# Kernel tuning notes

Hardware: AMD Instinct MI355X
Metric: run time of the kernel (lower is better)

## Reference

```python
import jax, jax.numpy as jnp
import numpy as np

B, T, D_MODEL = 4, 4096, 512
HEADS, BUCKET_SIZE, N_HASHES = 8, 64, 4
DIM_HEAD = D_MODEL // HEADS  # 64
D_FFN = 2048
N_BUCKETS = T // BUCKET_SIZE  # 64
SELF_ATTN_VALUE = -5e4  # reformer TOKEN_SELF_ATTN_VALUE


def setup_inputs() -> dict:
    key = jax.random.key(0)
    ks = jax.random.split(key, 16)
    s = 0.02
    return {
        'x': jax.random.normal(ks[0], (B, T, D_MODEL), jnp.float32),
        'rotations': jax.random.normal(ks[1], (DIM_HEAD, N_HASHES, N_BUCKETS // 2), jnp.float32),
        'w_qk': jax.random.normal(ks[2], (D_MODEL, D_MODEL), jnp.float32) * s,
        'w_v': jax.random.normal(ks[3], (D_MODEL, D_MODEL), jnp.float32) * s,
        'w_out': jax.random.normal(ks[4], (D_MODEL, D_MODEL), jnp.float32) * s,
        'b_out': jnp.zeros((D_MODEL,), jnp.float32),
        'ln1_g': jnp.ones((D_MODEL,), jnp.float32),
        'ln1_b': jnp.zeros((D_MODEL,), jnp.float32),
        'w1': jax.random.normal(ks[5], (D_FFN, D_MODEL), jnp.float32) * s,
        'b1': jnp.zeros((D_FFN,), jnp.float32),
        'w2': jax.random.normal(ks[6], (D_MODEL, D_FFN), jnp.float32) * s,
        'b2': jnp.zeros((D_MODEL,), jnp.float32),
        'ln2_g': jnp.ones((D_MODEL,), jnp.float32),
        'ln2_b': jnp.zeros((D_MODEL,), jnp.float32),
    }


def layer_norm(x, g, b, eps=1e-6):
    m = x.mean(-1, keepdims=True)
    v = ((x - m) ** 2).mean(-1, keepdims=True)
    return (x - m) / jnp.sqrt(v + eps) * g + b


def look_one_back(x):
    # concat each chunk with the previous chunk (wrap-around), along in-chunk axis
    prev = jnp.roll(x, 1, axis=1)
    return jnp.concatenate([x, prev], axis=2)


def lsh_attention(qk, v, rotations):
    # qk, v: (bh, t, d) with shared-QK; rotations: (d, n_hashes, n_buckets//2)
    bh, t, d = qk.shape
    # --- hash: random rotations, argmax over [R, -R] ---
    rot = jnp.einsum('btf,fhi->bhti', qk, rotations)
    rot = jnp.concatenate([rot, -rot], axis=-1)        # (bh, H, t, n_buckets)
    buckets = jnp.argmax(rot, axis=-1)                 # (bh, H, t)
    buckets = buckets + (jnp.arange(N_HASHES) * N_BUCKETS)[None, :, None]
    buckets = buckets.reshape(bh, N_HASHES * t)
    # --- sort by (bucket, position) ---
    ticker = jnp.arange(N_HASHES * t)
    buckets_and_t = t * buckets + (ticker % t)[None, :]
    sticker = jnp.argsort(buckets_and_t, axis=-1)      # stable sort
    undo_sort = jnp.argsort(sticker, axis=-1)
    st = sticker % t                                   # original positions, sorted order
    sqk = jnp.take_along_axis(qk, st[..., None], axis=1)
    sv = jnp.take_along_axis(v, st[..., None], axis=1)
    # --- chunk: n_hashes*n_buckets chunks of bucket_size tokens ---
    n_chunks = N_HASHES * N_BUCKETS
    bq_t = st.reshape(bh, n_chunks, -1)
    bqk = sqk.reshape(bh, n_chunks, -1, d)
    bv = sv.reshape(bh, n_chunks, -1, d)
    bk = bqk / jnp.clip(jnp.linalg.norm(bqk, axis=-1, keepdims=True), 1e-6, None)
    bk = look_one_back(bk)
    bv = look_one_back(bv)
    bkv_t = look_one_back(bq_t)
    # --- local attention within chunk (+ previous chunk) ---
    dots = jnp.einsum('bcid,bcjd->bcij', bqk, bk) * (DIM_HEAD ** -0.5)
    self_mask = bq_t[..., None] == bkv_t[..., None, :]
    dots = jnp.where(self_mask, SELF_ATTN_VALUE, dots)
    logits = jax.nn.logsumexp(dots, axis=-1, keepdims=True)
    probs = jnp.exp(dots - logits)
    bo = jnp.einsum('bcij,bcjd->bcid', probs, bv)
    # --- unsort and combine hash rounds by softmax over round logits ---
    so = bo.reshape(bh, N_HASHES * t, d)
    slogits = logits.reshape(bh, N_HASHES * t)
    o = jnp.take_along_axis(so, undo_sort[..., None], axis=1).reshape(bh, N_HASHES, t, d)
    lg = jnp.take_along_axis(slogits, undo_sort, axis=1).reshape(bh, N_HASHES, t, 1)
    w = jnp.exp(lg - jax.nn.logsumexp(lg, axis=1, keepdims=True))
    return (o * w).sum(axis=1)                         # (bh, t, d)


def reference(x, rotations, w_qk, w_v, w_out, b_out, ln1_g, ln1_b, w1, b1, w2, b2, ln2_g, ln2_b):
    b, t, _ = x.shape
    qk = x @ w_qk.T
    v = x @ w_v.T

    def split_heads(u):
        return u.reshape(b, t, HEADS, DIM_HEAD).transpose(0, 2, 1, 3).reshape(b * HEADS, t, DIM_HEAD)

    attn = lsh_attention(split_heads(qk), split_heads(v), rotations)
    attn = attn.reshape(b, HEADS, t, DIM_HEAD).transpose(0, 2, 1, 3).reshape(b, t, D_MODEL)
    attn = attn @ w_out.T + b_out
    # residual + LN (dropout is identity at inference)
    h = layer_norm(attn + x, ln1_g, ln1_b)
    # position-wise FFN with its own residual + LN
    f = jax.nn.relu(h @ w1.T + b1) @ w2.T + b2
    return layer_norm(f + h, ln2_g, ln2_b)
```

## Files before the change

### kernel.cpp

```cpp
#include <hip/hip_runtime.h>
#include <stdint.h>

typedef unsigned short u16;
typedef __attribute__((ext_vector_type(4))) int   i32x4;
typedef __attribute__((ext_vector_type(4))) float f32x4;

__device__ __forceinline__ u16 f2bf(float x){
  unsigned int u = __float_as_uint(x);
  u += 0x7FFFu + ((u >> 16) & 1u);
  return (u16)(u >> 16);
}
__device__ __forceinline__ float bf2f(u16 h){
  return __uint_as_float(((unsigned int)h) << 16);
}
__device__ __forceinline__ f32x4 mfma16(i32x4 a, i32x4 b, f32x4 c){
  asm("v_mfma_f32_16x16x32_bf16 %0, %1, %2, %0" : "+v"(c) : "v"(a), "v"(b));
  return c;
}
__device__ __forceinline__ f32x4 acc_fence(f32x4 c){
  asm volatile("s_nop 7\ns_nop 7" : "+v"(c));
  return c;
}
__device__ __forceinline__ void gl_lds16(const void* g, void* l){
  unsigned long long ga = (unsigned long long)g;
  unsigned int la = (unsigned int)(unsigned long long)l;
  __builtin_amdgcn_global_load_lds((const __attribute__((address_space(1))) void*)ga,
                                   (__attribute__((address_space(3))) void*)la, 16, 0, 0);
}
__device__ __forceinline__ int xcd_swz(int f, int n){
  int chunk = n >> 3;
  return (f & 7) * chunk + (f >> 3);
}
__device__ __forceinline__ unsigned int f2mono(float v){
  unsigned int u = __float_as_uint(v);
  return u ^ ((unsigned int)((int)u >> 31) | 0x80000000u);
}
__device__ __forceinline__ float mono2f(unsigned int mu){
  unsigned int u = (mu & 0x80000000u) ? (mu ^ 0x80000000u) : ~mu;
  return __uint_as_float(u);
}
__device__ __forceinline__ unsigned long long shfl_xor_u64(unsigned long long x, int m){
  int lo = __shfl_xor((int)(unsigned int)(x & 0xFFFFFFFFull), m);
  int hi = __shfl_xor((int)(unsigned int)(x >> 32), m);
  return ((unsigned long long)(unsigned int)hi << 32) | (unsigned int)lo;
}

__global__ __launch_bounds__(256) void k_cvt(const float* __restrict__ in, u16* __restrict__ out, int n4){
  int i = blockIdx.x*256 + threadIdx.x;
  if (i >= n4) return;
  float4 v = ((const float4*)in)[i];
  ushort4 o; o.x=f2bf(v.x); o.y=f2bf(v.y); o.z=f2bf(v.z); o.w=f2bf(v.w);
  ((ushort4*)out)[i] = o;
}
__global__ __launch_bounds__(256) void k_split(const float* __restrict__ in, u16* __restrict__ hi, u16* __restrict__ lo, int n4){
  int i = blockIdx.x*256 + threadIdx.x;
  if (i >= n4) return;
  float4 v = ((const float4*)in)[i];
  ushort4 h, l;
  h.x=f2bf(v.x); l.x=f2bf(v.x - bf2f(h.x));
  h.y=f2bf(v.y); l.y=f2bf(v.y - bf2f(h.y));
  h.z=f2bf(v.z); l.z=f2bf(v.z - bf2f(h.z));
  h.w=f2bf(v.w); l.w=f2bf(v.w - bf2f(h.w));
  ((ushort4*)hi)[i]=h; ((ushort4*)lo)[i]=l;
}
__global__ __launch_bounds__(256) void k_rotT(const float* __restrict__ rot, u16* __restrict__ hi, u16* __restrict__ lo){
  int i = blockIdx.x*256 + threadIdx.x;
  if (i >= 8192) return;
  int d = i & 63, n = i >> 6;
  float v = rot[d*128 + n];
  u16 h = f2bf(v);
  hi[i] = h; lo[i] = f2bf(v - bf2f(h));
}

template<int MODE>
__global__ __launch_bounds__(256) void k_gemm(
    const u16* __restrict__ A0, const u16* __restrict__ A1,
    const u16* __restrict__ B0, const u16* __restrict__ B1,
    const float* __restrict__ bias,
    float* __restrict__ Cf, u16* __restrict__ Cb,
    u16* __restrict__ Cb2, u16* __restrict__ Cb3,
    int M, int N, int K, int nterms)
{
  const int tid = threadIdx.x;
  const int l = tid & 63, w = tid >> 6;
  const int lr = l & 15, lg = l >> 4;
  int flat = blockIdx.y * gridDim.x + blockIdx.x;
  flat = xcd_swz(flat, gridDim.x * gridDim.y);
  const int m0 = (flat / gridDim.x) * 128, n0 = (flat % gridDim.x) * 128;
  const int mbase = (w >> 1) * 64, nbase = (w & 1) * 64;

  __shared__ __align__(16) u16 As[128*64];
  __shared__ __align__(16) u16 Bs[128*64];

  f32x4 zero = {0.f,0.f,0.f,0.f};
  f32x4 acc[4][4];
  #pragma unroll
  for (int i=0;i<4;i++)
    #pragma unroll
    for (int j=0;j<4;j++) acc[i][j] = zero;

  const int row_s = tid >> 3;
  const int c16   = tid & 7;

  for (int term = 0; term < nterms; ++term){
    const u16* Ap = (term==2) ? A1 : A0;
    const u16* Bp = (term==1) ? B1 : B0;
    for (int k0 = 0; k0 < K; k0 += 64){
      #pragma unroll
      for (int q=0;q<4;q++){
        int ra = q*32 + row_s;
        int cs = c16 ^ (ra & 7);
        gl_lds16(Ap + (size_t)(m0 + ra)*K + k0 + cs*8, (char*)As + q*4096 + tid*16);
        gl_lds16(Bp + (size_t)(n0 + ra)*K + k0 + cs*8, (char*)Bs + q*4096 + tid*16);
      }
      __syncthreads();
      #pragma unroll
      for (int kk=0; kk<64; kk+=32){
        i32x4 af[4], bfr[4];
        #pragma unroll
        for (int mf=0;mf<4;mf++){
          int row = mbase + mf*16 + lr;
          af[mf] = *(const i32x4*)((const char*)As + row*128 + (((kk*2) + (lg*16)) ^ ((row&7)<<4)));
        }
        #pragma unroll
        for (int nf=0;nf<4;nf++){
          int row = nbase + nf*16 + lr;
          bfr[nf] = *(const i32x4*)((const char*)Bs + row*128 + (((kk*2) + (lg*16)) ^ ((row&7)<<4)));
        }
        #pragma unroll
        for (int mf=0;mf<4;mf++)
          #pragma unroll
          for (int nf=0;nf<4;nf++)
            acc[mf][nf] = mfma16(af[mf], bfr[nf], acc[mf][nf]);
      }
      __syncthreads();
    }
  }

  if (MODE == 2){
    const int hh = (n0 + nbase) >> 6;
    #pragma unroll
    for (int mf=0;mf<4;mf++){
      f32x4 v[4];
      #pragma unroll
      for (int nf=0;nf<4;nf++) v[nf] = acc_fence(acc[mf][nf]);
      #pragma unroll
      for (int r=0;r<4;r++){
        float ss = 0.f;
        #pragma unroll
        for (int nf=0;nf<4;nf++) ss += v[nf][r]*v[nf][r];
        ss += __shfl_xor(ss, 1); ss += __shfl_xor(ss, 2);
        ss += __shfl_xor(ss, 4); ss += __shfl_xor(ss, 8);
        float scale = 1.f / fmaxf(sqrtf(ss), 1e-6f);
        int m = m0 + mbase + mf*16 + lg*4 + r;
        int b = m >> 12, t = m & 4095;
        size_t rowb = ((((size_t)(b*8 + hh)) << 12) + t) * 64;
        #pragma unroll
        for (int nf=0;nf<4;nf++){
          float val = v[nf][r];
          u16 hbf = f2bf(val);
          size_t idx = rowb + nf*16 + lr;
          Cb [idx] = hbf;
          Cb2[idx] = f2bf(val - bf2f(hbf));
          Cb3[idx] = f2bf(val * scale);
        }
      }
    }
    return;
  }

  #pragma unroll
  for (int mf=0;mf<4;mf++){
    #pragma unroll
    for (int nf=0;nf<4;nf++){
      f32x4 v = acc_fence(acc[mf][nf]);
      #pragma unroll
      for (int r=0;r<4;r++){
        int m = m0 + mbase + mf*16 + lg*4 + r;
        int n = n0 + nbase + nf*16 + lr;
        float val = v[r];
        if (MODE == 0){
          if (bias) val += bias[n];
          Cf[(size_t)m*N + n] = val;
        } else if (MODE == 1){
          val += bias[n];
          val = fmaxf(val, 0.f);
          Cb[(size_t)m*N + n] = f2bf(val);
        } else {
          int b = m >> 12, t = m & 4095, h = n >> 6, d = n & 63;
          size_t idx = ((((size_t)(b*8 + h)) << 12) + t)*64 + d;
          Cb[idx] = f2bf(val);
        }
      }
    }
  }
}

__global__ __launch_bounds__(256) void k_hash2(
    const u16* __restrict__ qh, const u16* __restrict__ ql,
    const u16* __restrict__ rh, const u16* __restrict__ rl,
    int* __restrict__ bkt)
{
  const int tid = threadIdx.x;
  const int l = tid & 63, w = tid >> 6, lr = l & 15, lg = l >> 4;
  __shared__ __align__(16) u16 Rh[128*64];
  __shared__ __align__(16) u16 Rl[128*64];
  {
    const int row_s = tid >> 3, c8 = tid & 7;
    #pragma unroll
    for (int q = 0; q < 4; q++){
      int ra = q*32 + row_s;
      int cs = c8 ^ (ra & 7);
      gl_lds16(rh + ra*64 + cs*8, (char*)Rh + q*4096 + tid*16);
      gl_lds16(rl + ra*64 + cs*8, (char*)Rl + q*4096 + tid*16);
    }
  }
  const int blk = xcd_swz(blockIdx.x, gridDim.x);
  const int qrow = blk*64 + w*16 + lr;
  const size_t qoff = (size_t)qrow*64;
  i32x4 qhf[2], qlf[2];
  qhf[0] = *(const i32x4*)(qh + qoff + lg*8);
  qhf[1] = *(const i32x4*)(qh + qoff + 32 + lg*8);
  qlf[0] = *(const i32x4*)(ql + qoff + lg*8);
  qlf[1] = *(const i32x4*)(ql + qoff + 32 + lg*8);
  __syncthreads();

  f32x4 zero = {0.f,0.f,0.f,0.f};
  f32x4 acc[8];
  #pragma unroll
  for (int i=0;i<8;i++) acc[i] = zero;
  #pragma unroll
  for (int ks = 0; ks < 2; ks++){
    #pragma unroll
    for (int nf = 0; nf < 8; nf++){
      int row = nf*16 + lr;
      int off = (ks*64 + lg*16) ^ ((row & 7) << 4);
      i32x4 rhf = *(const i32x4*)((const char*)Rh + row*128 + off);
      i32x4 rlf = *(const i32x4*)((const char*)Rl + row*128 + off);
      acc[nf] = mfma16(rhf, qhf[ks], acc[nf]);
      acc[nf] = mfma16(rlf, qhf[ks], acc[nf]);
      acc[nf] = mfma16(rhf, qlf[ks], acc[nf]);
    }
  }

  const int bh = qrow >> 12, t = qrow & 4095;
  #pragma unroll
  for (int hh = 0; hh < 4; hh++){
    f32x4 v0 = acc_fence(acc[2*hh]);
    f32x4 v1 = acc_fence(acc[2*hh+1]);
    unsigned long long kmax = 0, kmin = 0;
    #pragma unroll
    for (int r = 0; r < 4; r++){
      int j0 = lg*4 + r, j1 = 16 + lg*4 + r;
      unsigned int mu0 = f2mono(v0[r]), mu1 = f2mono(v1[r]);
      unsigned long long a = ((unsigned long long)mu0 << 32) | (unsigned int)(31 - j0);
      unsigned long long b = ((unsigned long long)mu1 << 32) | (unsigned int)(31 - j1);
      if (a > kmax) kmax = a;
      if (b > kmax) kmax = b;
      unsigned long long c = ((unsigned long long)(~mu0) << 32) | (unsigned int)(31 - j0);
      unsigned long long d = ((unsigned long long)(~mu1) << 32) | (unsigned int)(31 - j1);
      if (c > kmin) kmin = c;
      if (d > kmin) kmin = d;
    }
    #pragma unroll
    for (int msk = 16; msk < 64; msk <<= 1){
      unsigned long long o1 = shfl_xor_u64(kmax, msk); if (o1 > kmax) kmax = o1;
      unsigned long long o2 = shfl_xor_u64(kmin, msk); if (o2 > kmin) kmin = o2;
    }
    if (lg == 0){
      float vmax = mono2f((unsigned int)(kmax >> 32));
      int jmax = 31 - (int)(kmax & 0xFFFFFFFFull);
      float vmin = mono2f(~(unsigned int)(kmin >> 32));
      int jmin = 31 - (int)(kmin & 0xFFFFFFFFull);
      int bucket = (vmax >= -vmin) ? jmax : 32 + jmin;
      bkt[((size_t)(bh*4 + hh) << 12) + t] = bucket;
    }
  }
}

__global__ __launch_bounds__(64) void k_sort(const int* __restrict__ buckets, int* __restrict__ st){
  const int grp = blockIdx.x;
  const int t = threadIdx.x;
  __shared__ int hist[64][65];
  __shared__ int tot[64];
  const size_t gbase = ((size_t)grp) << 12;
  #pragma unroll
  for (int b=0;b<64;b++) hist[t][b] = 0;
  __syncthreads();
  for (int i=0;i<64;i++){
    int b = buckets[gbase + t*64 + i];
    hist[t][b]++;
  }
  __syncthreads();
  { int run = 0;
    for (int tt=0; tt<64; tt++){ int v = hist[tt][t]; hist[tt][t] = run; run += v; }
    tot[t] = run; }
  __syncthreads();
  { int v = tot[t]; int incl = v;
    #pragma unroll
    for (int d=1; d<64; d<<=1){ int n = __shfl_up(incl, d, 64); if (t >= d) incl += n; }
    tot[t] = incl - v; }
  __syncthreads();
  const size_t obase = (((size_t)(grp>>2)) << 14) + ((size_t)(grp&3) << 12);
  for (int i=0;i<64;i++){
    int e = t*64 + i;
    int b = buckets[gbase + e];
    int dest = tot[b] + hist[t][b];
    hist[t][b]++;
    st[obase + dest] = e;
  }
}

__global__ __launch_bounds__(256, 4) void k_attn(
    const u16* __restrict__ qb, const u16* __restrict__ kn, const u16* __restrict__ vB,
    const int* __restrict__ st, float* __restrict__ lgt_out, u16* __restrict__ bo)
{
  int flat = blockIdx.y * gridDim.x + blockIdx.x;
  flat = xcd_swz(flat, gridDim.x * gridDim.y);
  const int c = flat & 255, bh = flat >> 8;
  const int rnd = c >> 6;
  const int tid = threadIdx.x;
  const int l = tid & 63, w = tid >> 6, lr = l & 15, lg = l >> 4;

  __shared__ __align__(16) u16 Ks[128*64];
  __shared__ __align__(16) u16 Vt[64][136];
  __shared__ int posk[128];

  if (tid < 128){
    int cc = (tid < 64) ? c : ((c + 255) & 255);
    posk[tid] = st[(((size_t)bh) << 14) + (cc << 6) + (tid & 63)];
  }
  __syncthreads();

  const size_t kvbase = ((size_t)bh) << 12;

  {
    const int rsub = l >> 3, c8 = l & 7;
    #pragma unroll
    for (int q2 = 0; q2 < 4; q2++){
      int row = w*32 + q2*8 + rsub;
      int cs = c8 ^ (row & 7);
      gl_lds16(kn + (kvbase + posk[row])*64 + cs*8,
               (char*)Ks + (w*4 + q2)*1024 + l*16);
    }
  }

  const int pos_q16 = posk[w*16 + lr];
  i32x4 qf[2];
  #pragma unroll
  for (int ks = 0; ks < 2; ks++)
    qf[ks] = *(const i32x4*)(qb + (kvbase + pos_q16)*64 + ks*32 + lg*8);

  {
    const int pp = tid & 63, db = tid >> 6;
    const int q5 = pp & 15;
    const int K0 = (pp >> 4)*32 + 16*((q5 >> 1) & 1) + 4*(q5 >> 2) + 2*(q5 & 1);
    const u16* r0 = vB + (kvbase + posk[K0])*64 + db*16;
    const u16* r1 = vB + (kvbase + posk[K0+1])*64 + db*16;
    uint4 a0 = *(const uint4*)r0, a1 = *(const uint4*)(r0 + 8);
    uint4 b0 = *(const uint4*)r1, b1 = *(const uint4*)(r1 + 8);
    uint av[8] = {a0.x,a0.y,a0.z,a0.w,a1.x,a1.y,a1.z,a1.w};
    uint bv[8] = {b0.x,b0.y,b0.z,b0.w,b1.x,b1.y,b1.z,b1.w};
    #pragma unroll
    for (int dd = 0; dd < 16; dd++){
      uint lo = (av[dd>>1] >> ((dd&1)*16)) & 0xFFFFu;
      uint hi = (bv[dd>>1] >> ((dd&1)*16)) & 0xFFFFu;
      *(uint*)((char*)&Vt[db*16 + dd][0] + pp*4) = lo | (hi << 16);
    }
  }
  __syncthreads();

  f32x4 zero = {0.f,0.f,0.f,0.f};
  f32x4 s[8];
  #pragma unroll
  for (int i=0;i<8;i++) s[i] = zero;
  #pragma unroll
  for (int ks = 0; ks < 2; ks++){
    #pragma unroll
    for (int nf = 0; nf < 8; nf++){
      int row = nf*16 + lr;
      i32x4 kf = *(const i32x4*)((const char*)Ks + row*128 + ((ks*64 + lg*16) ^ ((row&7)<<4)));
      s[nf] = mfma16(kf, qf[ks], s[nf]);
    }
  }

  float sv[8][4];
  const int q_loc = w*16 + lr;
  #pragma unroll
  for (int nf=0;nf<8;nf++){
    f32x4 t = acc_fence(s[nf]);
    #pragma unroll
    for (int r=0;r<4;r++){
      int k = nf*16 + lg*4 + r;
      sv[nf][r] = (k == q_loc) ? -5e4f : t[r]*0.125f;
    }
  }
  float m = -1e30f;
  #pragma unroll
  for (int nf=0;nf<8;nf++)
    #pragma unroll
    for (int r=0;r<4;r++) m = fmaxf(m, sv[nf][r]);
  m = fmaxf(m, __shfl_xor(m, 16));
  m = fmaxf(m, __shfl_xor(m, 32));
  float sum = 0.f;
  #pragma unroll
  for (int nf=0;nf<8;nf++)
    #pragma unroll
    for (int r=0;r<4;r++){ sv[nf][r] = __expf(sv[nf][r] - m); sum += sv[nf][r]; }
  sum += __shfl_xor(sum, 16);
  sum += __shfl_xor(sum, 32);
  float lv = m + logf(sum);
  float inv = 1.f / sum;
  if (l < 16)
    lgt_out[(((size_t)(bh*4 + rnd)) << 12) + pos_q16] = lv;

  i32x4 pa[4];
  #pragma unroll
  for (int ks=0;ks<4;ks++){
    uint wd[4];
    #pragma unroll
    for (int h2=0; h2<2; h2++){
      int nf = 2*ks + h2;
      float p0 = sv[nf][0]*inv, p1 = sv[nf][1]*inv;
      float p2 = sv[nf][2]*inv, p3 = sv[nf][3]*inv;
      wd[h2*2]   = (uint)f2bf(p0) | ((uint)f2bf(p1)<<16);
      wd[h2*2+1] = (uint)f2bf(p2) | ((uint)f2bf(p3)<<16);
    }
    i32x4 t = {(int)wd[0],(int)wd[1],(int)wd[2],(int)wd[3]};
    pa[ks] = t;
  }

  f32x4 o[4];
  #pragma unroll
  for (int i=0;i<4;i++) o[i] = zero;
  #pragma unroll
  for (int ks=0;ks<4;ks++){
    #pragma unroll
    for (int nf=0;nf<4;nf++){
      i32x4 vf = *(const i32x4*)((const char*)&Vt[nf*16 + lr][0] + ks*64 + lg*16);
      o[nf] = mfma16(pa[ks], vf, o[nf]);
    }
  }
  #pragma unroll
  for (int nf=0;nf<4;nf++){
    f32x4 ov = acc_fence(o[nf]);
    #pragma unroll
    for (int r=0;r<4;r++){
      int q = w*16 + lg*4 + r;
      bo[((((size_t)(bh*4 + rnd)) << 12) + posk[q])*64 + nf*16 + lr] = f2bf(ov[r]);
    }
  }
}

__global__ __launch_bounds__(256) void k_combine(const u16* __restrict__ bo, const float* __restrict__ lgt,
                                                 u16* __restrict__ attn){
  const int wid = blockIdx.x * 4 + (threadIdx.x >> 6);
  const int l = threadIdx.x & 63;
  const int bh = wid >> 12, t = wid & 4095;
  const size_t lbase = (((size_t)bh) << 14) + t;
  float l0 = lgt[lbase], l1 = lgt[lbase + 4096], l2 = lgt[lbase + 8192], l3 = lgt[lbase + 12288];
  float m = fmaxf(fmaxf(l0,l1), fmaxf(l2,l3));
  float w0 = __expf(l0-m), w1 = __expf(l1-m), w2 = __expf(l2-m), w3 = __expf(l3-m);
  float inv = 1.f / (w0+w1+w2+w3);
  const size_t bbase = ((((size_t)bh) << 14) + t) * 64 + l;
  float o = w0 * bf2f(bo[bbase])
          + w1 * bf2f(bo[bbase + (size_t)4096*64])
          + w2 * bf2f(bo[bbase + (size_t)8192*64])
          + w3 * bf2f(bo[bbase + (size_t)12288*64]);
  o *= inv;
  int b = bh >> 3, h = bh & 7;
  attn[((((size_t)b) << 12) + t) * 512 + h*64 + l] = f2bf(o);
}

template<int WB16>
__global__ __launch_bounds__(256) void k_ln(const float* __restrict__ a, const float* __restrict__ res,
                                            const float* __restrict__ g, const float* __restrict__ bb,
                                            float* __restrict__ of, u16* __restrict__ ob){
  const int row = blockIdx.x*4 + (threadIdx.x >> 6);
  const int l = threadIdx.x & 63;
  const size_t base = (size_t)row*512 + l*8;
  float4 a0 = *(const float4*)(a + base);
  float4 a1 = *(const float4*)(a + base + 4);
  float4 r0 = *(const float4*)(res + base);
  float4 r1 = *(const float4*)(res + base + 4);
  float v[8] = {a0.x+r0.x, a0.y+r0.y, a0.z+r0.z, a0.w+r0.w,
                a1.x+r1.x, a1.y+r1.y, a1.z+r1.z, a1.w+r1.w};
  float sum = 0.f;
  #pragma unroll
  for (int j=0;j<8;j++) sum += v[j];
  #pragma unroll
  for (int msk=1; msk<64; msk<<=1) sum += __shfl_xor(sum, msk);
  float mean = sum * (1.f/512.f);
  float ss = 0.f;
  #pragma unroll
  for (int j=0;j<8;j++){ float d = v[j]-mean; ss += d*d; }
  #pragma unroll
  for (int msk=1; msk<64; msk<<=1) ss += __shfl_xor(ss, msk);
  float rstd = rsqrtf(ss * (1.f/512.f) + 1e-6f);
  float4 g0 = *(const float4*)(g + l*8),  g1 = *(const float4*)(g + l*8 + 4);
  float4 b0 = *(const float4*)(bb + l*8), b1 = *(const float4*)(bb + l*8 + 4);
  float gv[8] = {g0.x,g0.y,g0.z,g0.w,g1.x,g1.y,g1.z,g1.w};
  float bv[8] = {b0.x,b0.y,b0.z,b0.w,b1.x,b1.y,b1.z,b1.w};
  float y[8];
  #pragma unroll
  for (int j=0;j<8;j++) y[j] = (v[j]-mean)*rstd*gv[j] + bv[j];
  #pragma unroll
  for (int j=0;j<8;j++) of[base+j] = y[j];
  if (WB16){
    #pragma unroll
    for (int j=0;j<8;j++) ob[base+j] = f2bf(y[j]);
  }
}

extern "C" void kernel_launch(void* const* d_in, const int* in_sizes, int n_in,
                              void* d_out, int out_size, void* d_ws, size_t ws_size,
                              hipStream_t stream) {
  const float* x     = (const float*)d_in[0];
  const float* rot   = (const float*)d_in[1];
  const float* w_qk  = (const float*)d_in[2];
  const float* w_v   = (const float*)d_in[3];
  const float* w_out = (const float*)d_in[4];
  const float* b_out = (const float*)d_in[5];
  const float* ln1_g = (const float*)d_in[6];
  const float* ln1_b = (const float*)d_in[7];
  const float* w1    = (const float*)d_in[8];
  const float* b1    = (const float*)d_in[9];
  const float* w2    = (const float*)d_in[10];
  const float* b2    = (const float*)d_in[11];
  const float* ln2_g = (const float*)d_in[12];
  const float* ln2_b = (const float*)d_in[13];
  float* out = (float*)d_out;

  char* p = (char*)d_ws;
  u16*   xh   = (u16*)(p);
  u16*   xl   = (u16*)(p + 16777216);
  u16*   wqkh = (u16*)(p + 33554432);
  u16*   wqkl = (u16*)(p + 34078720);
  u16*   wvb  = (u16*)(p + 34603008);
  u16*   wob  = (u16*)(p + 35127296);
  u16*   w1b  = (u16*)(p + 35651584);
  u16*   w2b  = (u16*)(p + 37748736);
  u16*   qbuf = (u16*)(p + 39845888);
  u16*   knb  = (u16*)(p + 56623104);
  u16*   vb   = (u16*)(p + 73400320);
  int*   bkt  = (int*)(p + 90177536);
  int*   stb  = (int*)(p + 92274688);
  float* lgt  = (float*)(p + 94371840);
  u16*   bo   = (u16*)(p + 96468992);
  u16*   qlo   = bo;
  u16*   rothi = wqkh;
  u16*   rotlo = wqkl;
  u16*   attnc = xl;
  float* hf    = (float*)(p + 39845888);
  u16*   hb    = xh;
  u16*   hid   = bo;

  k_split<<<8192, 256, 0, stream>>>(x, xh, xl, 16384*512/4);
  k_split<<<256,  256, 0, stream>>>(w_qk, wqkh, wqkl, 512*512/4);
  k_cvt  <<<256,  256, 0, stream>>>(w_v,   wvb, 512*512/4);
  k_cvt  <<<256,  256, 0, stream>>>(w_out, wob, 512*512/4);
  k_cvt  <<<1024, 256, 0, stream>>>(w1, w1b, 2048*512/4);
  k_cvt  <<<1024, 256, 0, stream>>>(w2, w2b, 2048*512/4);

  k_gemm<2><<<dim3(4,128), 256, 0, stream>>>(xh, xl, wqkh, wqkl, nullptr, nullptr, qbuf, qlo, knb, 16384, 512, 512, 3);
  k_gemm<3><<<dim3(4,128), 256, 0, stream>>>(xh, nullptr, wvb, nullptr, nullptr, nullptr, vb, nullptr, nullptr, 16384, 512, 512, 1);
  k_rotT<<<32, 256, 0, stream>>>(rot, rothi, rotlo);
  k_hash2<<<2048, 256, 0, stream>>>(qbuf, qlo, rothi, rotlo, bkt);
  k_sort<<<128, 64, 0, stream>>>(bkt, stb);
  k_attn<<<dim3(256,32), 256, 0, stream>>>(qbuf, knb, vb, stb, lgt, bo);
  k_combine<<<32768, 256, 0, stream>>>(bo, lgt, attnc);
  k_gemm<0><<<dim3(4,128), 256, 0, stream>>>(attnc, nullptr, wob, nullptr, b_out, out, nullptr, nullptr, nullptr, 16384, 512, 512, 1);
  k_ln<1><<<4096, 256, 0, stream>>>(out, x, ln1_g, ln1_b, hf, hb);
  k_gemm<1><<<dim3(16,128), 256, 0, stream>>>(hb, nullptr, w1b, nullptr, b1, nullptr, hid, nullptr, nullptr, 16384, 2048, 512, 1);
  k_gemm<0><<<dim3(4,128), 256, 0, stream>>>(hid, nullptr, w2b, nullptr, b2, out, nullptr, nullptr, nullptr, 16384, 512, 2048, 1);
  k_ln<0><<<4096, 256, 0, stream>>>(out, hf, ln2_g, ln2_b, out, nullptr);
}
```

Measured before the change: 333.9 us.

## Fuse split-bf16 QK GEMM terms, stage sort buckets in LDS, streamline attention softmax

Several separate changes. The three-term split-bf16 QK projection moves into a dedicated kernel that loads hi/lo A and B tiles once and issues the three MFMAs per tile together, instead of looping over terms and reloading tiles. The sort kernel stages bucket ids in LDS with coalesced loads rather than strided global reads. The attention kernel folds the 1/8 scale into the normalized key and drops the max subtraction, relying on bounded cosine logits. It also defers the 1/sum normalization to after the PV MFMA, uses packed bf16 conversion instructions, and raises wave priority around MFMA blocks. The cost is extra LDS in the QK GEMM, which may lower occupancy.

Result: faster. 315.0 us (-5.7%).

```diff
diff --git a/kernel.cpp b/kernel.cpp
--- a/kernel.cpp
+++ b/kernel.cpp
@@ -12,6 +12,11 @@
 }
 __device__ __forceinline__ float bf2f(u16 h){
   return __uint_as_float(((unsigned int)h) << 16);
+}
+__device__ __forceinline__ unsigned int cvtpk_bf16(float lo, float hi){
+  unsigned int r;
+  asm("v_cvt_pk_bf16_f32 %0, %1, %2" : "=v"(r) : "v"(lo), "v"(hi));
+  return r;
 }
 __device__ __forceinline__ f32x4 mfma16(i32x4 a, i32x4 b, f32x4 c){
   asm("v_mfma_f32_16x16x32_bf16 %0, %1, %2, %0" : "+v"(c) : "v"(a), "v"(b));
@@ -74,12 +79,10 @@
 
 template<int MODE>
 __global__ __launch_bounds__(256) void k_gemm(
-    const u16* __restrict__ A0, const u16* __restrict__ A1,
-    const u16* __restrict__ B0, const u16* __restrict__ B1,
+    const u16* __restrict__ A0, const u16* __restrict__ B0,
     const float* __restrict__ bias,
     float* __restrict__ Cf, u16* __restrict__ Cb,
-    u16* __restrict__ Cb2, u16* __restrict__ Cb3,
-    int M, int N, int K, int nterms)
+    int M, int N, int K)
 {
   const int tid = threadIdx.x;
   const int l = tid & 63, w = tid >> 6;
@@ -102,71 +105,35 @@
   const int row_s = tid >> 3;
   const int c16   = tid & 7;
 
-  for (int term = 0; term < nterms; ++term){
-    const u16* Ap = (term==2) ? A1 : A0;
-    const u16* Bp = (term==1) ? B1 : B0;
-    for (int k0 = 0; k0 < K; k0 += 64){
-      #pragma unroll
-      for (int q=0;q<4;q++){
-        int ra = q*32 + row_s;
-        int cs = c16 ^ (ra & 7);
-        gl_lds16(Ap + (size_t)(m0 + ra)*K + k0 + cs*8, (char*)As + q*4096 + tid*16);
-        gl_lds16(Bp + (size_t)(n0 + ra)*K + k0 + cs*8, (char*)Bs + q*4096 + tid*16);
+  for (int k0 = 0; k0 < K; k0 += 64){
+    #pragma unroll
+    for (int q=0;q<4;q++){
+      int ra = q*32 + row_s;
+      int cs = c16 ^ (ra & 7);
+      gl_lds16(A0 + (size_t)(m0 + ra)*K + k0 + cs*8, (char*)As + q*4096 + tid*16);
+      gl_lds16(B0 + (size_t)(n0 + ra)*K + k0 + cs*8, (char*)Bs + q*4096 + tid*16);
+    }
+    __syncthreads();
+    #pragma unroll
+    for (int kk=0; kk<64; kk+=32){
+      i32x4 af[4], bfr[4];
+      #pragma unroll
+      for (int mf=0;mf<4;mf++){
+        int row = mbase + mf*16 + lr;
+        af[mf] = *(const i32x4*)((const char*)As + row*128 + (((kk*2) + (lg*16)) ^ ((row&7)<<4)));
       }
-      __syncthreads();
-      #pragma unroll
-      for (int kk=0; kk<64; kk+=32){
-        i32x4 af[4], bfr[4];
+      #pragma unroll
+      for (int nf=0;nf<4;nf++){
+        int row = nbase + nf*16 + lr;
+        bfr[nf] = *(const i32x4*)((const char*)Bs + row*128 + (((kk*2) + (lg*16)) ^ ((row&7)<<4)));
+      }
+      #pragma unroll
+      for (int mf=0;mf<4;mf++)
         #pragma unroll
-        for (int mf=0;mf<4;mf++){
-          int row = mbase + mf*16 + lr;
-          af[mf] = *(const i32x4*)((const char*)As + row*128 + (((kk*2) + (lg*16)) ^ ((row&7)<<4)));
-        }
-        #pragma unroll
-        for (int nf=0;nf<4;nf++){
-          int row = nbase + nf*16 + lr;
-          bfr[nf] = *(const i32x4*)((const char*)Bs + row*128 + (((kk*2) + (lg*16)) ^ ((row&7)<<4)));
-        }
-        #pragma unroll
-        for (int mf=0;mf<4;mf++)
-          #pragma unroll
-          for (int nf=0;nf<4;nf++)
-            acc[mf][nf] = mfma16(af[mf], bfr[nf], acc[mf][nf]);
-      }
-      __syncthreads();
-    }
-  }
-
-  if (MODE == 2){
-    const int hh = (n0 + nbase) >> 6;
-    #pragma unroll
-    for (int mf=0;mf<4;mf++){
-      f32x4 v[4];
-      #pragma unroll
-      for (int nf=0;nf<4;nf++) v[nf] = acc_fence(acc[mf][nf]);
-      #pragma unroll
-      for (int r=0;r<4;r++){
-        float ss = 0.f;
-        #pragma unroll
-        for (int nf=0;nf<4;nf++) ss += v[nf][r]*v[nf][r];
-        ss += __shfl_xor(ss, 1); ss += __shfl_xor(ss, 2);
-        ss += __shfl_xor(ss, 4); ss += __shfl_xor(ss, 8);
-        float scale = 1.f / fmaxf(sqrtf(ss), 1e-6f);
-        int m = m0 + mbase + mf*16 + lg*4 + r;
-        int b = m >> 12, t = m & 4095;
-        size_t rowb = ((((size_t)(b*8 + hh)) << 12) + t) * 64;
-        #pragma unroll
-        for (int nf=0;nf<4;nf++){
-          float val = v[nf][r];
-          u16 hbf = f2bf(val);
-          size_t idx = rowb + nf*16 + lr;
-          Cb [idx] = hbf;
-          Cb2[idx] = f2bf(val - bf2f(hbf));
-          Cb3[idx] = f2bf(val * scale);
-        }
-      }
-    }
-    return;
+        for (int nf=0;nf<4;nf++)
+          acc[mf][nf] = mfma16(af[mf], bfr[nf], acc[mf][nf]);
+    }
+    __syncthreads();
   }
 
   #pragma unroll
@@ -196,6 +163,107 @@
   }
 }
 
+__global__ __launch_bounds__(256) void k_gemmqk(
+    const u16* __restrict__ Ah, const u16* __restrict__ Al,
+    const u16* __restrict__ Bh, const u16* __restrict__ Bl,
+    u16* __restrict__ qb, u16* __restrict__ qlo, u16* __restrict__ kn)
+{
+  const int K = 512;
+  const int tid = threadIdx.x;
+  const int l = tid & 63, w = tid >> 6;
+  const int lr = l & 15, lg = l >> 4;
+  int flat = blockIdx.y * gridDim.x + blockIdx.x;
+  flat = xcd_swz(flat, gridDim.x * gridDim.y);
+  const int m0 = (flat >> 2) * 128, n0 = (flat & 3) * 128;
+  const int mbase = (w >> 1) * 64, nbase = (w & 1) * 64;
+
+  __shared__ __align__(16) u16 AsH[128*64];
+  __shared__ __align__(16) u16 AsL[128*64];
+  __shared__ __align__(16) u16 BsH[128*64];
+  __shared__ __align__(16) u16 BsL[128*64];
+
+  f32x4 zero = {0.f,0.f,0.f,0.f};
+  f32x4 acc[4][4];
+  #pragma unroll
+  for (int i=0;i<4;i++)
+    #pragma unroll
+    for (int j=0;j<4;j++) acc[i][j] = zero;
+
+  const int row_s = tid >> 3;
+  const int c16   = tid & 7;
+
+  for (int k0 = 0; k0 < K; k0 += 64){
+    #pragma unroll
+    for (int q=0;q<4;q++){
+      int ra = q*32 + row_s;
+      int cs = c16 ^ (ra & 7);
+      size_t ao = (size_t)(m0 + ra)*K + k0 + cs*8;
+      size_t bo = (size_t)(n0 + ra)*K + k0 + cs*8;
+      gl_lds16(Ah + ao, (char*)AsH + q*4096 + tid*16);
+      gl_lds16(Al + ao, (char*)AsL + q*4096 + tid*16);
+      gl_lds16(Bh + bo, (char*)BsH + q*4096 + tid*16);
+      gl_lds16(Bl + bo, (char*)BsL + q*4096 + tid*16);
+    }
+    __syncthreads();
+    #pragma unroll
+    for (int kk=0; kk<64; kk+=32){
+      i32x4 ah[4], al[4], bh2[4], bl2[4];
+      #pragma unroll
+      for (int mf=0;mf<4;mf++){
+        int row = mbase + mf*16 + lr;
+        int off = (((kk*2) + (lg*16)) ^ ((row&7)<<4));
+        ah[mf] = *(const i32x4*)((const char*)AsH + row*128 + off);
+        al[mf] = *(const i32x4*)((const char*)AsL + row*128 + off);
+      }
+      #pragma unroll
+      for (int nf=0;nf<4;nf++){
+        int row = nbase + nf*16 + lr;
+        int off = (((kk*2) + (lg*16)) ^ ((row&7)<<4));
+        bh2[nf] = *(const i32x4*)((const char*)BsH + row*128 + off);
+        bl2[nf] = *(const i32x4*)((const char*)BsL + row*128 + off);
+      }
+      #pragma unroll
+      for (int mf=0;mf<4;mf++)
+        #pragma unroll
+        for (int nf=0;nf<4;nf++){
+          acc[mf][nf] = mfma16(ah[mf], bh2[nf], acc[mf][nf]);
+          acc[mf][nf] = mfma16(al[mf], bh2[nf], acc[mf][nf]);
+          acc[mf][nf] = mfma16(ah[mf], bl2[nf], acc[mf][nf]);
+        }
+    }
+    __syncthreads();
+  }
+
+  const int hh = (n0 + nbase) >> 6;
+  #pragma unroll
+  for (int mf=0;mf<4;mf++){
+    f32x4 v[4];
+    #pragma unroll
+    for (int nf=0;nf<4;nf++) v[nf] = acc_fence(acc[mf][nf]);
+    #pragma unroll
+    for (int r=0;r<4;r++){
+      float ss = 0.f;
+      #pragma unroll
+      for (int nf=0;nf<4;nf++) ss += v[nf][r]*v[nf][r];
+      ss += __shfl_xor(ss, 1); ss += __shfl_xor(ss, 2);
+      ss += __shfl_xor(ss, 4); ss += __shfl_xor(ss, 8);
+      float scale = 0.125f / fmaxf(sqrtf(ss), 1e-6f);
+      int m = m0 + mbase + mf*16 + lg*4 + r;
+      int b = m >> 12, t = m & 4095;
+      size_t rowb = ((((size_t)(b*8 + hh)) << 12) + t) * 64;
+      #pragma unroll
+      for (int nf=0;nf<4;nf++){
+        float val = v[nf][r];
+        u16 hbf = f2bf(val);
+        size_t idx = rowb + nf*16 + lr;
+        qb [idx] = hbf;
+        qlo[idx] = f2bf(val - bf2f(hbf));
+        kn [idx] = f2bf(val * scale);
+      }
+    }
+  }
+}
+
 __global__ __launch_bounds__(256) void k_hash2(
     const u16* __restrict__ qh, const u16* __restrict__ ql,
     const u16* __restrict__ rh, const u16* __restrict__ rl,
@@ -281,14 +349,17 @@
 __global__ __launch_bounds__(64) void k_sort(const int* __restrict__ buckets, int* __restrict__ st){
   const int grp = blockIdx.x;
   const int t = threadIdx.x;
+  __shared__ int bkL[4096];
   __shared__ int hist[64][65];
   __shared__ int tot[64];
   const size_t gbase = ((size_t)grp) << 12;
+  for (int i=0;i<64;i++)
+    bkL[i*64 + t] = buckets[gbase + i*64 + t];
   #pragma unroll
   for (int b=0;b<64;b++) hist[t][b] = 0;
   __syncthreads();
   for (int i=0;i<64;i++){
-    int b = buckets[gbase + t*64 + i];
+    int b = bkL[t*64 + i];
     hist[t][b]++;
   }
   __syncthreads();
@@ -304,7 +375,7 @@
   const size_t obase = (((size_t)(grp>>2)) << 14) + ((size_t)(grp&3) << 12);
   for (int i=0;i<64;i++){
     int e = t*64 + i;
-    int b = buckets[gbase + e];
+    int b = bkL[e];
     int dest = tot[b] + hist[t][b];
     hist[t][b]++;
     st[obase + dest] = e;
@@ -374,6 +445,7 @@
   f32x4 s[8];
   #pragma unroll
   for (int i=0;i<8;i++) s[i] = zero;
+  __builtin_amdgcn_s_setprio(1);
   #pragma unroll
   for (int ks = 0; ks < 2; ks++){
     #pragma unroll
@@ -383,33 +455,25 @@
       s[nf] = mfma16(kf, qf[ks], s[nf]);
     }
   }
-
-  float sv[8][4];
+  __builtin_amdgcn_s_setprio(0);
+
+  float p[8][4];
   const int q_loc = w*16 + lr;
+  float sum = 0.f;
   #pragma unroll
   for (int nf=0;nf<8;nf++){
     f32x4 t = acc_fence(s[nf]);
     #pragma unroll
     for (int r=0;r<4;r++){
       int k = nf*16 + lg*4 + r;
-      sv[nf][r] = (k == q_loc) ? -5e4f : t[r]*0.125f;
-    }
-  }
-  float m = -1e30f;
-  #pragma unroll
-  for (int nf=0;nf<8;nf++)
-    #pragma unroll
-    for (int r=0;r<4;r++) m = fmaxf(m, sv[nf][r]);
-  m = fmaxf(m, __shfl_xor(m, 16));
-  m = fmaxf(m, __shfl_xor(m, 32));
-  float sum = 0.f;
-  #pragma unroll
-  for (int nf=0;nf<8;nf++)
-    #pragma unroll
-    for (int r=0;r<4;r++){ sv[nf][r] = __expf(sv[nf][r] - m); sum += sv[nf][r]; }
+      float e = (k == q_loc) ? 0.f : __expf(t[r]);
+      p[nf][r] = e;
+      sum += e;
+    }
+  }
   sum += __shfl_xor(sum, 16);
   sum += __shfl_xor(sum, 32);
-  float lv = m + logf(sum);
+  float lv = logf(sum);
   float inv = 1.f / sum;
   if (l < 16)
     lgt_out[(((size_t)(bh*4 + rnd)) << 12) + pos_q16] = lv;
@@ -417,22 +481,18 @@
   i32x4 pa[4];
   #pragma unroll
   for (int ks=0;ks<4;ks++){
-    uint wd[4];
-    #pragma unroll
-    for (int h2=0; h2<2; h2++){
-      int nf = 2*ks + h2;
-      float p0 = sv[nf][0]*inv, p1 = sv[nf][1]*inv;
-      float p2 = sv[nf][2]*inv, p3 = sv[nf][3]*inv;
-      wd[h2*2]   = (uint)f2bf(p0) | ((uint)f2bf(p1)<<16);
-      wd[h2*2+1] = (uint)f2bf(p2) | ((uint)f2bf(p3)<<16);
-    }
-    i32x4 t = {(int)wd[0],(int)wd[1],(int)wd[2],(int)wd[3]};
+    uint w0 = cvtpk_bf16(p[2*ks][0],   p[2*ks][1]);
+    uint w1 = cvtpk_bf16(p[2*ks][2],   p[2*ks][3]);
+    uint w2 = cvtpk_bf16(p[2*ks+1][0], p[2*ks+1][1]);
+    uint w3 = cvtpk_bf16(p[2*ks+1][2], p[2*ks+1][3]);
+    i32x4 t = {(int)w0,(int)w1,(int)w2,(int)w3};
     pa[ks] = t;
   }
 
   f32x4 o[4];
   #pragma unroll
   for (int i=0;i<4;i++) o[i] = zero;
+  __builtin_amdgcn_s_setprio(1);
   #pragma unroll
   for (int ks=0;ks<4;ks++){
     #pragma unroll
@@ -441,13 +501,17 @@
       o[nf] = mfma16(pa[ks], vf, o[nf]);
     }
   }
+  __builtin_amdgcn_s_setprio(0);
+  float invq[4];
+  #pragma unroll
+  for (int r=0;r<4;r++) invq[r] = __shfl(inv, lg*4 + r, 64);
   #pragma unroll
   for (int nf=0;nf<4;nf++){
     f32x4 ov = acc_fence(o[nf]);
     #pragma unroll
     for (int r=0;r<4;r++){
       int q = w*16 + lg*4 + r;
-      bo[((((size_t)(bh*4 + rnd)) << 12) + posk[q])*64 + nf*16 + lr] = f2bf(ov[r]);
+      bo[((((size_t)(bh*4 + rnd)) << 12) + posk[q])*64 + nf*16 + lr] = f2bf(ov[r] * invq[r]);
     }
   }
 }
@@ -562,16 +626,16 @@
   k_cvt  <<<1024, 256, 0, stream>>>(w1, w1b, 2048*512/4);
   k_cvt  <<<1024, 256, 0, stream>>>(w2, w2b, 2048*512/4);
 
-  k_gemm<2><<<dim3(4,128), 256, 0, stream>>>(xh, xl, wqkh, wqkl, nullptr, nullptr, qbuf, qlo, knb, 16384, 512, 512, 3);
-  k_gemm<3><<<dim3(4,128), 256, 0, stream>>>(xh, nullptr, wvb, nullptr, nullptr, nullptr, vb, nullptr, nullptr, 16384, 512, 512, 1);
+  k_gemmqk<<<dim3(4,128), 256, 0, stream>>>(xh, xl, wqkh, wqkl, qbuf, qlo, knb);
+  k_gemm<3><<<dim3(4,128), 256, 0, stream>>>(xh, wvb, nullptr, nullptr, vb, 16384, 512, 512);
   k_rotT<<<32, 256, 0, stream>>>(rot, rothi, rotlo);
   k_hash2<<<2048, 256, 0, stream>>>(qbuf, qlo, rothi, rotlo, bkt);
   k_sort<<<128, 64, 0, stream>>>(bkt, stb);
   k_attn<<<dim3(256,32), 256, 0, stream>>>(qbuf, knb, vb, stb, lgt, bo);
   k_combine<<<32768, 256, 0, stream>>>(bo, lgt, attnc);
-  k_gemm<0><<<dim3(4,128), 256, 0, stream>>>(attnc, nullptr, wob, nullptr, b_out, out, nullptr, nullptr, nullptr, 16384, 512, 512, 1);
+  k_gemm<0><<<dim3(4,128), 256, 0, stream>>>(attnc, wob, b_out, out, nullptr, 16384, 512, 512);
   k_ln<1><<<4096, 256, 0, stream>>>(out, x, ln1_g, ln1_b, hf, hb);
-  k_gemm<1><<<dim3(16,128), 256, 0, stream>>>(hb, nullptr, w1b, nullptr, b1, nullptr, hid, nullptr, nullptr, 16384, 2048, 512, 1);
-  k_gemm<0><<<dim3(4,128), 256, 0, stream>>>(hid, nullptr, w2b, nullptr, b2, out, nullptr, nullptr, nullptr, 16384, 512, 2048, 1);
+  k_gemm<1><<<dim3(16,128), 256, 0, stream>>>(hb, w1b, b1, nullptr, hid, 16384, 2048, 512);
+  k_gemm<0><<<dim3(4,128), 256, 0, stream>>>(hid, w2b, b2, out, nullptr, 16384, 512, 2048);
   k_ln<0><<<4096, 256, 0, stream>>>(out, hf, ln2_g, ln2_b, out, nullptr);
 }
```
